# Kernel tuning notes

Measured on AMD Instinct MI355X. Metric: run time of the kernel, lower is better.

The kernel has to match this reference:

```python
import jax, jax.numpy as jnp
import numpy as np

NUM_ANGLES = 90


def _hough_tables(H, W, num_angles):
    """Precompute bilinear rho-bin tables, matching the torch buffers."""
    thetas = jnp.linspace(0.0, np.pi * (1.0 - 1.0 / num_angles), num_angles)
    max_rho = int(np.ceil(np.sqrt(H ** 2 + W ** 2)))
    num_rhos = 2 * max_rho + 1
    rho_min, rho_max = float(-max_rho), float(max_rho)
    ys = jnp.arange(H, dtype=jnp.float32) - H / 2
    xs = jnp.arange(W, dtype=jnp.float32) - W / 2
    yy, xx = jnp.meshgrid(ys, xs, indexing='ij')  # [H, W]
    # rho_map: [A, H, W]
    rho_map = (xx[None] * jnp.cos(thetas)[:, None, None]
               + yy[None] * jnp.sin(thetas)[:, None, None])
    rho_norm = (rho_map - rho_min) / (rho_max - rho_min) * (num_rhos - 1)
    rho_norm = rho_norm.reshape(num_angles, -1)  # [A, HW]
    # torch .long() truncates; values are >=0 up to fp error, clamp handles edges
    rho_floor = jnp.clip(rho_norm.astype(jnp.int32), 0, num_rhos - 2)
    rho_frac = rho_norm - rho_floor.astype(jnp.float32)
    rho_ceil = jnp.clip(rho_floor + 1, 0, num_rhos - 1)
    return rho_floor, rho_frac, rho_ceil, num_rhos


def setup_inputs() -> dict:
    key = jax.random.key(0)
    B, H, W = 16, 256, 256
    mask = jax.random.uniform(key, (B, 1, H, W), dtype=jnp.float32)
    return {"mask": mask}


def reference(mask) -> jnp.ndarray:
    B, _, H, W = mask.shape
    A = NUM_ANGLES
    rho_floor, rho_frac, rho_ceil, R = _hough_tables(H, W, A)

    mask_flat = mask.reshape(B, -1).astype(jnp.float32)          # [B, HW]
    w_floor = (1.0 - rho_frac)[None] * mask_flat[:, None, :]     # [B, A, HW]
    w_ceil = rho_frac[None] * mask_flat[:, None, :]              # [B, A, HW]

    b_idx = jnp.arange(B)[:, None, None]   # [B,1,1]
    a_idx = jnp.arange(A)[None, :, None]   # [1,A,1]
    hough = jnp.zeros((B, A, R), dtype=jnp.float32)
    hough = hough.at[b_idx, a_idx, rho_floor[None]].add(w_floor)
    hough = hough.at[b_idx, a_idx, rho_ceil[None]].add(w_ceil)
    return hough
```

## Files before the change

### kernel.cpp

```cpp
#include <hip/hip_runtime.h>
#include <math.h>

#define NUM_A 90
#define RBINS 727
#define HDIM  256
#define WDIM  256
#define RMIN  181
#define RACT  365
#define TPB   768
#define PH_ROWS 52
#define ROWSTR  260
#define NPH     5
#define TILE_N  (PH_ROWS * ROWSTR)

__global__ void angles_k(float* __restrict__ tab) {
    int a = threadIdx.x;
    if (a < NUM_A) {
        double th = (double)a * (3.14159265358979323846 / 90.0);
        tab[2 * a]     = (float)cos(th);
        tab[2 * a + 1] = (float)sin(th);
    }
}

__global__ __launch_bounds__(256) void transpose_k(const float* __restrict__ in,
                                                   float* __restrict__ out) {
    __shared__ float tile[32][33];
    int b = blockIdx.z;
    const float* ib = in  + (size_t)b * (HDIM * WDIM);
    float*       ob = out + (size_t)b * (HDIM * WDIM);
    int x0 = blockIdx.x * 32, y0 = blockIdx.y * 32;
    int tx = threadIdx.x, ty = threadIdx.y;
#pragma unroll
    for (int j = ty; j < 32; j += 8)
        tile[j][tx] = ib[(size_t)(y0 + j) * WDIM + (x0 + tx)];
    __syncthreads();
#pragma unroll
    for (int j = ty; j < 32; j += 8)
        ob[(size_t)(x0 + j) * HDIM + (y0 + tx)] = tile[tx][j];
}

static __device__ __forceinline__ float tap3(float f0, float lo, float ci,
                                             float onems, float onepls,
                                             float v0, float v1, float v2,
                                             float acc) {
    float fr = f0 - lo;
    float a0 = fmaf(fr, -ci, onems), b0 = fmaf(fr, ci, onepls);
    acc = fmaf(v0, __builtin_amdgcn_fmed3f(a0, b0, 0.0f), acc);
    float a1 = a0 - ci, b1 = b0 + ci;
    acc = fmaf(v1, __builtin_amdgcn_fmed3f(a1, b1, 0.0f), acc);
    float a2 = a1 - ci, b2 = b1 + ci;
    acc = fmaf(v2, __builtin_amdgcn_fmed3f(a2, b2, 0.0f), acc);
    return acc;
}

__global__ __launch_bounds__(TPB, 6) void hough_lds_k(const float* __restrict__ srcA,
                                                      const float* __restrict__ srcB,
                                                      const float* __restrict__ tab,
                                                      float* __restrict__ out) {
    __shared__ float tile[TILE_N];
    int ba = blockIdx.x;
    int b  = ba / NUM_A;
    int a  = ba - b * NUM_A;

    float c = tab[2 * a], s = tab[2 * a + 1];
    bool  xs = fabsf(c) >= fabsf(s);
    float ci = xs ? c : s;
    float cj = xs ? s : c;
    const float* src = (xs ? srcA : srcB) + (size_t)b * (HDIM * WDIM);

    int   tid = threadIdx.x;
    int   bin = tid >> 1;
    int   m   = tid & 1;
    int   r   = RMIN + bin;
    float rf  = (float)r;
    bool  active = bin < RACT;

    float p = fminf(-128.0f * ci, 127.0f * ci);
    float q = fmaxf(-128.0f * ci, 127.0f * ci);
    int jl, jh;
    float acj = fabsf(cj);
    if (acj > 1e-5f) {
        float invj = 1.0f / cj;
        float jA = (rf + 1.0f - p - 363.0f) * invj + 128.0f;
        float jB = (rf - 1.0f - q - 363.0f) * invj + 128.0f;
        float jmn = fminf(jA, jB) - 1.0f;
        float jmx = fmaxf(jA, jB) + 2.0f;
        jl = (int)fminf(fmaxf(jmn, 0.0f), 256.0f);
        jh = (int)fminf(fmaxf(jmx, 0.0f), 256.0f);
    } else {
        bool any = (363.0f + q > rf - 1.01f) && (363.0f + p < rf + 1.01f);
        jl = 0; jh = any ? 256 : 0;
    }
    if (!active) { jl = 0; jh = 0; }

    int start = jl + ((jl ^ m) & 1);

    float inv  = 1.0f / ci;
    float sgn  = (ci > 0.0f) ? -1.0f : 1.0f;
    float Z0   = 363.0f - rf - 128.0f * cj - 128.0f * ci;
    float LO0  = (sgn - Z0) * inv;
    float dlo  = -cj * inv;
    float onems = 1.0f - sgn;
    float onepls = 1.0f + sgn;
    float dlo2 = dlo + dlo;

    int wid = tid >> 6, lane = tid & 63;
    float acc = 0.0f;
    for (int ph = 0; ph < NPH; ++ph) {
        int phb   = ph * PH_ROWS;
        int nrows = (phb + PH_ROWS <= 256) ? PH_ROWS : (256 - phb);
        if (ph) __syncthreads();
        for (int sl = wid; sl < nrows; sl += 12) {
            const float* grow = src + (size_t)(phb + sl) * 256 + lane * 4;
            float* lrow = tile + sl * ROWSTR + lane * 4;
            __builtin_amdgcn_global_load_lds(
                (const __attribute__((address_space(1))) unsigned int*)grow,
                (__attribute__((address_space(3))) unsigned int*)lrow, 16, 0, 0);
        }
        __syncthreads();

        int pstart = phb + ((phb ^ m) & 1);
        int jsp = start > pstart ? start : pstart;
        int jep = jh < phb + nrows ? jh : phb + nrows;
        if (jep <= jsp) continue;
        int cnt = (jep - jsp + 1) >> 1;

        float lo = fmaf((float)jsp, dlo, LO0);
        int rowf = (jsp - phb) * ROWSTR;
        int k = 0;
        int npair = cnt >> 1;
        for (int pr = 0; pr < npair; ++pr, k += 2) {
            float lo0 = lo;
            float lo1 = lo + dlo2;
            lo = lo1 + dlo2;
            float f0 = __builtin_amdgcn_fmed3f(ceilf(lo0), 0.0f, 253.0f);
            float f1 = __builtin_amdgcn_fmed3f(ceilf(lo1), 0.0f, 253.0f);
            int i0 = (int)f0, i1 = (int)f1;
            const float* p0 = tile + rowf + i0;
            const float* p1 = tile + rowf + 2 * ROWSTR + i1;
            rowf += 4 * ROWSTR;
            float v00 = p0[0], v01 = p0[1], v02 = p0[2];
            float v10 = p1[0], v11 = p1[1], v12 = p1[2];
            acc = tap3(f0, lo0, ci, onems, onepls, v00, v01, v02, acc);
            acc = tap3(f1, lo1, ci, onems, onepls, v10, v11, v12, acc);
        }
        if (cnt & 1) {
            float f0 = __builtin_amdgcn_fmed3f(ceilf(lo), 0.0f, 253.0f);
            int   i0 = (int)f0;
            const float* p0 = tile + rowf + i0;
            float v00 = p0[0], v01 = p0[1], v02 = p0[2];
            acc = tap3(f0, lo, ci, onems, onepls, v00, v01, v02, acc);
        }
    }

    acc += __shfl_xor(acc, 1);
    if (active && m == 0)
        out[(size_t)ba * RBINS + r] = acc;
}

typedef float f3v __attribute__((ext_vector_type(3)));
typedef f3v __attribute__((aligned(4))) f3u;
#define FB_GRP (368 * 4)

__global__ __launch_bounds__(256) void hough_fb_k(const float* __restrict__ src0,
                                                  float* __restrict__ out, int nba) {
    int gtid = blockIdx.x * 256 + threadIdx.x;
    int grp  = gtid / FB_GRP;
    if (grp >= nba) return;
    int k    = gtid - grp * FB_GRP;
    int ba   = __builtin_amdgcn_readfirstlane(grp);
    int b    = ba / NUM_A;
    int a    = ba - b * NUM_A;
    double th = (double)a * (3.14159265358979323846 / 90.0);
    float c = (float)cos(th), s = (float)sin(th);
    bool  xs = fabsf(c) >= fabsf(s);
    float ci = xs ? c : s, cj = xs ? s : c;
    const float* src = src0 + (size_t)b * (HDIM * WDIM);
    int   bin = k >> 2, m = k & 3;
    int   r = RMIN + bin;
    float rf = (float)r;
    bool  active = bin < RACT;
    float inv = 1.0f / ci, ainv = fabsf(inv);
    float p = fminf(-128.0f * ci, 127.0f * ci);
    float q = fmaxf(-128.0f * ci, 127.0f * ci);
    int jl, jh;
    float acj = fabsf(cj);
    if (acj > 1e-5f) {
        float invj = 1.0f / cj;
        float jA = (rf + 1.0f - p - 363.0f) * invj + 128.0f;
        float jB = (rf - 1.0f - q - 363.0f) * invj + 128.0f;
        jl = (int)fminf(fmaxf(fminf(jA, jB) - 1.0f, 0.0f), 256.0f);
        jh = (int)fminf(fmaxf(fmaxf(jA, jB) + 2.0f, 0.0f), 256.0f);
    } else {
        bool any = (363.0f + q > rf - 1.01f) && (363.0f + p < rf + 1.01f);
        jl = 0; jh = any ? 256 : 0;
    }
    if (!active) { jl = 0; jh = 0; }
    int len = jh - jl;
    int js = jl + ((m * len) >> 2);
    int je = jl + (((m + 1) * len) >> 2);
    float dlo = -cj * inv;
    float LO0 = 128.0f + (rf - 363.0f) * inv - ainv + 128.0f * cj * inv;
    float Z0  = 363.0f - rf - 128.0f * cj - 128.0f * ci;
    float ci2 = ci + ci;
    float acc = 0.0f;
    for (int j = js; j < je; ++j) {
        float jf  = (float)j;
        float lo0 = fmaf(jf, dlo, LO0);
        float z0  = fmaf(jf, cj, Z0);
        float f0  = __builtin_amdgcn_fmed3f(ceilf(lo0), 0.0f, 253.0f);
        int   i0  = (int)f0;
        float a0, b0, c0;
        if (xs) {
            f3v mm = *(const f3u*)(src + ((size_t)j << 8) + i0);
            a0 = mm.x; b0 = mm.y; c0 = mm.z;
        } else {
            const float* p0 = src + j + ((size_t)i0 << 8);
            a0 = p0[0]; b0 = p0[256]; c0 = p0[512];
        }
        float u0 = fmaf(f0, ci, z0);
        acc = fmaf(a0, fmaxf(1.0f - fabsf(u0), 0.0f), acc);
        acc = fmaf(b0, fmaxf(1.0f - fabsf(u0 + ci), 0.0f), acc);
        acc = fmaf(c0, fmaxf(1.0f - fabsf(u0 + ci2), 0.0f), acc);
    }
    acc += __shfl_xor(acc, 1);
    acc += __shfl_xor(acc, 2);
    if (active && m == 0)
        out[(size_t)ba * RBINS + r] = acc;
}

extern "C" void kernel_launch(void* const* d_in, const int* in_sizes, int n_in,
                              void* d_out, int out_size, void* d_ws, size_t ws_size,
                              hipStream_t stream) {
    const float* mask = (const float*)d_in[0];
    float* out = (float*)d_out;
    int B = in_sizes[0] / (HDIM * WDIM);
    int nba = B * NUM_A;

    size_t needT = (size_t)B * HDIM * WDIM * sizeof(float);
    size_t needW = needT + 2 * NUM_A * sizeof(float);
    int fast = (d_ws != nullptr && ws_size >= needW) ? 1 : 0;
    float* maskT = (float*)d_ws;
    float* tab   = (float*)((char*)d_ws + needT);

    hipMemsetAsync(d_out, 0, (size_t)out_size * sizeof(float), stream);

    if (fast) {
        transpose_k<<<dim3(WDIM / 32, HDIM / 32, B), dim3(32, 8), 0, stream>>>(mask, maskT);
        angles_k<<<1, 128, 0, stream>>>(tab);
        hough_lds_k<<<nba, TPB, 0, stream>>>(mask, maskT, tab, out);
    } else {
        int nthreads = nba * FB_GRP;
        hough_fb_k<<<(nthreads + 255) / 256, 256, 0, stream>>>(mask, out, nba);
    }
}
```

Before: 74.37 us.

## Compute two adjacent rho bins per thread group sharing a 5-wide LDS window

```diff
diff --git a/kernel.cpp b/kernel.cpp
--- a/kernel.cpp
+++ b/kernel.cpp
@@ -7,6 +7,7 @@
 #define WDIM  256
 #define RMIN  181
 #define RACT  365
+#define RMAX  545
 #define TPB   768
 #define PH_ROWS 52
 #define ROWSTR  260
@@ -69,43 +70,47 @@
     const float* src = (xs ? srcA : srcB) + (size_t)b * (HDIM * WDIM);
 
     int   tid = threadIdx.x;
-    int   bin = tid >> 1;
-    int   m   = tid & 1;
-    int   r   = RMIN + bin;
-    float rf  = (float)r;
-    bool  active = bin < RACT;
+    int   pp  = tid >> 2;
+    int   m   = tid & 3;
+    int   r0  = RMIN + 2 * pp;
+    int   r1  = r0 + 1;
+    bool  act = (r0 <= RMAX);
 
     float p = fminf(-128.0f * ci, 127.0f * ci);
     float q = fmaxf(-128.0f * ci, 127.0f * ci);
+    float rlo = (float)r0 - 1.0f, rhi = (float)r1 + 1.0f;
     int jl, jh;
     float acj = fabsf(cj);
     if (acj > 1e-5f) {
         float invj = 1.0f / cj;
-        float jA = (rf + 1.0f - p - 363.0f) * invj + 128.0f;
-        float jB = (rf - 1.0f - q - 363.0f) * invj + 128.0f;
+        float jA = (rhi - p - 363.0f) * invj + 128.0f;
+        float jB = (rlo - q - 363.0f) * invj + 128.0f;
         float jmn = fminf(jA, jB) - 1.0f;
         float jmx = fmaxf(jA, jB) + 2.0f;
         jl = (int)fminf(fmaxf(jmn, 0.0f), 256.0f);
         jh = (int)fminf(fmaxf(jmx, 0.0f), 256.0f);
     } else {
-        bool any = (363.0f + q > rf - 1.01f) && (363.0f + p < rf + 1.01f);
+        bool any = (363.0f + q > rlo) && (363.0f + p < rhi);
         jl = 0; jh = any ? 256 : 0;
     }
-    if (!active) { jl = 0; jh = 0; }
-
-    int start = jl + ((jl ^ m) & 1);
+    if (!act) { jl = 0; jh = 0; }
 
     float inv  = 1.0f / ci;
     float sgn  = (ci > 0.0f) ? -1.0f : 1.0f;
-    float Z0   = 363.0f - rf - 128.0f * cj - 128.0f * ci;
-    float LO0  = (sgn - Z0) * inv;
+    int   irA  = (inv > 0.0f) ? r0 : r1;
+    int   irB  = (inv > 0.0f) ? r1 : r0;
+    float rAf  = (float)irA;
+    float LOA0 = (sgn - (363.0f - rAf - 128.0f * cj - 128.0f * ci)) * inv;
     float dlo  = -cj * inv;
+    float ainv = fabsf(inv);
     float onems = 1.0f - sgn;
     float onepls = 1.0f + sgn;
-    float dlo2 = dlo + dlo;
+    float dlo4 = 4.0f * dlo;
+
+    int start = jl + ((m - jl) & 3);
 
     int wid = tid >> 6, lane = tid & 63;
-    float acc = 0.0f;
+    float accA = 0.0f, accB = 0.0f;
     for (int ph = 0; ph < NPH; ++ph) {
         int phb   = ph * PH_ROWS;
         int nrows = (phb + PH_ROWS <= 256) ? PH_ROWS : (256 - phb);
@@ -119,43 +124,75 @@
         }
         __syncthreads();
 
-        int pstart = phb + ((phb ^ m) & 1);
+        int pstart = phb + ((m - phb) & 3);
         int jsp = start > pstart ? start : pstart;
         int jep = jh < phb + nrows ? jh : phb + nrows;
         if (jep <= jsp) continue;
-        int cnt = (jep - jsp + 1) >> 1;
-
-        float lo = fmaf((float)jsp, dlo, LO0);
+        int cnt = (jep - jsp + 3) >> 2;
+
+        float loA = fmaf((float)jsp, dlo, LOA0);
         int rowf = (jsp - phb) * ROWSTR;
-        int k = 0;
         int npair = cnt >> 1;
-        for (int pr = 0; pr < npair; ++pr, k += 2) {
-            float lo0 = lo;
-            float lo1 = lo + dlo2;
-            lo = lo1 + dlo2;
-            float f0 = __builtin_amdgcn_fmed3f(ceilf(lo0), 0.0f, 253.0f);
-            float f1 = __builtin_amdgcn_fmed3f(ceilf(lo1), 0.0f, 253.0f);
-            int i0 = (int)f0, i1 = (int)f1;
-            const float* p0 = tile + rowf + i0;
-            const float* p1 = tile + rowf + 2 * ROWSTR + i1;
-            rowf += 4 * ROWSTR;
-            float v00 = p0[0], v01 = p0[1], v02 = p0[2];
-            float v10 = p1[0], v11 = p1[1], v12 = p1[2];
-            acc = tap3(f0, lo0, ci, onems, onepls, v00, v01, v02, acc);
-            acc = tap3(f1, lo1, ci, onems, onepls, v10, v11, v12, acc);
+        for (int pr = 0; pr < npair; ++pr) {
+            float lo0 = loA;
+            float lo1 = loA + dlo4;
+            loA = lo1 + dlo4;
+            float lb0 = lo0 + ainv;
+            float fA0 = __builtin_amdgcn_fmed3f(ceilf(lo0), 0.0f, 253.0f);
+            float fB0 = __builtin_amdgcn_fmed3f(ceilf(lb0), 0.0f, 253.0f);
+            int iA0 = (int)fA0, iB0 = (int)fB0;
+            const float* P0 = tile + rowf + iA0;
+            float x0 = P0[0], x1 = P0[1], x2 = P0[2], x3 = P0[3], x4 = P0[4];
+            float lb1 = lo1 + ainv;
+            float fA1 = __builtin_amdgcn_fmed3f(ceilf(lo1), 0.0f, 253.0f);
+            float fB1 = __builtin_amdgcn_fmed3f(ceilf(lb1), 0.0f, 253.0f);
+            int iA1 = (int)fA1, iB1 = (int)fB1;
+            const float* P1 = tile + rowf + 4 * ROWSTR + iA1;
+            float y0 = P1[0], y1 = P1[1], y2 = P1[2], y3 = P1[3], y4 = P1[4];
+            rowf += 8 * ROWSTR;
+
+            int d0 = iB0 - iA0;
+            bool d01 = d0 >= 1, d02 = d0 >= 2;
+            float s00 = d01 ? x1 : x0; s00 = d02 ? x2 : s00;
+            float s01 = d01 ? x2 : x1; s01 = d02 ? x3 : s01;
+            float s02 = d01 ? x3 : x2; s02 = d02 ? x4 : s02;
+            accA = tap3(fA0, lo0, ci, onems, onepls, x0, x1, x2, accA);
+            accB = tap3(fB0, lb0, ci, onems, onepls, s00, s01, s02, accB);
+
+            int d1 = iB1 - iA1;
+            bool d11 = d1 >= 1, d12 = d1 >= 2;
+            float s10 = d11 ? y1 : y0; s10 = d12 ? y2 : s10;
+            float s11 = d11 ? y2 : y1; s11 = d12 ? y3 : s11;
+            float s12 = d11 ? y3 : y2; s12 = d12 ? y4 : s12;
+            accA = tap3(fA1, lo1, ci, onems, onepls, y0, y1, y2, accA);
+            accB = tap3(fB1, lb1, ci, onems, onepls, s10, s11, s12, accB);
         }
         if (cnt & 1) {
-            float f0 = __builtin_amdgcn_fmed3f(ceilf(lo), 0.0f, 253.0f);
-            int   i0 = (int)f0;
-            const float* p0 = tile + rowf + i0;
-            float v00 = p0[0], v01 = p0[1], v02 = p0[2];
-            acc = tap3(f0, lo, ci, onems, onepls, v00, v01, v02, acc);
-        }
-    }
-
-    acc += __shfl_xor(acc, 1);
-    if (active && m == 0)
-        out[(size_t)ba * RBINS + r] = acc;
+            float lb = loA + ainv;
+            float fA = __builtin_amdgcn_fmed3f(ceilf(loA), 0.0f, 253.0f);
+            float fB = __builtin_amdgcn_fmed3f(ceilf(lb), 0.0f, 253.0f);
+            int iA = (int)fA, iB = (int)fB;
+            const float* P0 = tile + rowf + iA;
+            float x0 = P0[0], x1 = P0[1], x2 = P0[2], x3 = P0[3], x4 = P0[4];
+            int d = iB - iA;
+            bool dd1 = d >= 1, dd2 = d >= 2;
+            float s0 = dd1 ? x1 : x0; s0 = dd2 ? x2 : s0;
+            float s1 = dd1 ? x2 : x1; s1 = dd2 ? x3 : s1;
+            float s2 = dd1 ? x3 : x2; s2 = dd2 ? x4 : s2;
+            accA = tap3(fA, loA, ci, onems, onepls, x0, x1, x2, accA);
+            accB = tap3(fB, lb, ci, onems, onepls, s0, s1, s2, accB);
+        }
+    }
+
+    accA += __shfl_xor(accA, 1);
+    accA += __shfl_xor(accA, 2);
+    accB += __shfl_xor(accB, 1);
+    accB += __shfl_xor(accB, 2);
+    if (m == 0) {
+        float* o = out + (size_t)ba * RBINS;
+        if (irA <= RMAX && act) o[irA] = accA;
+        if (irB <= RMAX && act) o[irB] = accB;
+    }
 }
 
 typedef float f3v __attribute__((ext_vector_type(3)));
```

Result: slower. 86.95 us (+16.9%).
